# Optimization experiments

Measured on AMD Instinct MI355X. Metric: run time of the kernel, lower is better.

The kernel has to match this reference:

```python
import jax, jax.numpy as jnp
import numpy as np

D_IN = 2048
D_OUT = 2048
NUM_HEADS = 16
HEAD_DIM = D_OUT // NUM_HEADS


def setup_inputs() -> dict:
    key = jax.random.key(0)
    ks = jax.random.split(key, 6)
    b, t = 2, 2048
    x = jax.random.normal(ks[0], (b, t, D_IN), dtype=jnp.float32)
    s = 0.02
    Wq = jax.random.normal(ks[1], (D_OUT, D_IN), dtype=jnp.float32) * s
    Wk = jax.random.normal(ks[2], (D_OUT, D_IN), dtype=jnp.float32) * s
    Wv = jax.random.normal(ks[3], (D_OUT, D_IN), dtype=jnp.float32) * s
    Wo = jax.random.normal(ks[4], (D_OUT, D_OUT), dtype=jnp.float32) * s
    bo = jnp.zeros((D_OUT,), dtype=jnp.float32)
    theta = (10000.0 ** (-jnp.arange(0, HEAD_DIM, 2, dtype=jnp.float32) / HEAD_DIM))
    return {"x": x, "Wq": Wq, "Wk": Wk, "Wv": Wv, "Wo": Wo, "bo": bo, "theta": theta}


def _rope(v, sin, cos):
    # v: [b, t, h, d]; split even/odd feature indices, rotate, concat halves
    ve, vo = v[..., ::2], v[..., 1::2]
    return jnp.concatenate([ve * cos - vo * sin, ve * sin + vo * cos], axis=-1)


def reference(x, Wq, Wk, Wv, Wo, bo, theta):
    b, t, _ = x.shape
    q = (x @ Wq.T).reshape(b, t, NUM_HEADS, HEAD_DIM)
    k = (x @ Wk.T).reshape(b, t, NUM_HEADS, HEAD_DIM)
    v = (x @ Wv.T).reshape(b, t, NUM_HEADS, HEAD_DIM)

    pos = jnp.arange(t, dtype=jnp.float32)[:, None]          # [t, 1]
    freq = pos * theta[None, :]                              # [t, d/2]
    sin = jnp.sin(freq)[None, :, None, :]                    # [1, t, 1, d/2]
    cos = jnp.cos(freq)[None, :, None, :]
    q = _rope(q, sin, cos)
    k = _rope(k, sin, cos)

    # [b, h, t, t]
    scores = jnp.einsum('bqhd,bkhd->bhqk', q, k)
    causal = jnp.triu(jnp.ones((t, t), dtype=bool), k=1)
    scores = jnp.where(causal[None, None], -jnp.inf, scores)
    attn = jax.nn.softmax(scores / jnp.sqrt(jnp.float32(HEAD_DIM)), axis=-1)

    ctx = jnp.einsum('bhqk,bkhd->bqhd', attn, v).reshape(b, t, D_OUT)
    return ctx @ Wo.T + bo
```

## Files before the change

### kernel.cpp

```cpp
#include <hip/hip_runtime.h>

typedef unsigned short ushortT;
typedef short short8 __attribute__((ext_vector_type(8)));
typedef float floatx4 __attribute__((ext_vector_type(4)));

#define D_MODEL 2048
#define HEAD_DIM 128
#define NUM_HEADS 16
#define SEQ 2048
#define BATCH 2
#define M_TOK (BATCH * SEQ)
#define QKV_ELEMS ((size_t)M_TOK * D_MODEL)
#define W_ELEMS ((size_t)D_MODEL * D_MODEL)

__device__ __forceinline__ float bf2f(ushortT h) {
    return __uint_as_float(((unsigned int)h) << 16);
}
__device__ __forceinline__ ushortT f2bf(float f) {
    unsigned int u = __float_as_uint(f);
    u = u + 0x7fffu + ((u >> 16) & 1u);
    return (ushortT)(u >> 16);
}

__device__ __forceinline__ void gload_lds16(const ushortT* g, short* lds_wave_base) {
    __builtin_amdgcn_global_load_lds(
        (const __attribute__((address_space(1))) unsigned int*)g,
        (__attribute__((address_space(3))) unsigned int*)lds_wave_base,
        16, 0, 0);
}

__global__ __launch_bounds__(256) void cvt_all(
    const float* __restrict__ x,  const float* __restrict__ wq,
    const float* __restrict__ wk, const float* __restrict__ wv,
    const float* __restrict__ wo,
    ushortT* __restrict__ xb,  ushortT* __restrict__ wqb,
    ushortT* __restrict__ wkb, ushortT* __restrict__ wvb,
    ushortT* __restrict__ wob)
{
    const size_t XC = QKV_ELEMS / 8;
    const size_t WC = W_ELEMS / 8;
    size_t c = (size_t)blockIdx.x * 256 + threadIdx.x;
    const float* s; ushortT* d;
    if (c < XC)              { s = x;  d = xb;  }
    else if ((c -= XC) < WC) { s = wq; d = wqb; }
    else if ((c -= WC) < WC) { s = wk; d = wkb; }
    else if ((c -= WC) < WC) { s = wv; d = wvb; }
    else     { c -= WC;        s = wo; d = wob; }
    const float* f = s + c * 8;
    floatx4 a = *(const floatx4*)f;
    floatx4 b = *(const floatx4*)(f + 4);
    short8 r;
    r[0] = (short)f2bf(a.x); r[1] = (short)f2bf(a.y);
    r[2] = (short)f2bf(a.z); r[3] = (short)f2bf(a.w);
    r[4] = (short)f2bf(b.x); r[5] = (short)f2bf(b.y);
    r[6] = (short)f2bf(b.z); r[7] = (short)f2bf(b.w);
    *(short8*)(d + c * 8) = r;
}

__global__ __launch_bounds__(256) void sincos_kernel(
    float* __restrict__ tbl, const float* __restrict__ theta)
{
    const int p = blockIdx.x * 256 + threadIdx.x;
    const int t = p >> 6, d = p & 63;
    const float ang = (float)t * theta[d];
    tbl[2 * p]     = sinf(ang);
    tbl[2 * p + 1] = cosf(ang);
}

template<bool OUTF32>
__global__ __launch_bounds__(256) void gemm_bt(
    const ushortT* __restrict__ A,
    const ushortT* __restrict__ W0, const ushortT* __restrict__ W1,
    const ushortT* __restrict__ W2,
    void* C0, void* C1, void* C2, const float* __restrict__ bias)
{
    __shared__ short As[128 * 32];
    __shared__ short Bs[128 * 32];

    const int z = blockIdx.z;
    const ushortT* W = (z == 0) ? W0 : (z == 1 ? W1 : W2);
    void* C = (z == 0) ? C0 : (z == 1 ? C1 : C2);

    const int tid  = threadIdx.x;
    const int wave = tid >> 6;
    const int lane = tid & 63;
    const int lr   = lane & 15;
    const int quad = lane >> 4;
    const int wm   = (wave & 1) * 64;
    const int wn   = (wave >> 1) * 64;

    const int blockM = blockIdx.y * 128;
    const int blockN = blockIdx.x * 128;

    const int srow = tid >> 2;
    const int scol = (tid & 3) * 8;
    const ushortT* ag = A + (size_t)(blockM + srow) * D_MODEL + scol;
    const ushortT* wg = W + (size_t)(blockN + srow) * D_MODEL + scol;
    short* al = As + wave * 512;
    short* bl = Bs + wave * 512;

    floatx4 acc[4][4];
    #pragma unroll
    for (int i = 0; i < 4; i++)
        #pragma unroll
        for (int j = 0; j < 4; j++) acc[i][j] = (floatx4){0.f, 0.f, 0.f, 0.f};

    for (int kk = 0; kk < D_MODEL; kk += 32) {
        gload_lds16(ag + kk,                 al);
        gload_lds16(ag + kk + 64 * D_MODEL,  al + 64 * 32);
        gload_lds16(wg + kk,                 bl);
        gload_lds16(wg + kk + 64 * D_MODEL,  bl + 64 * 32);
        __syncthreads();

        short8 af[4], bf[4];
        #pragma unroll
        for (int s = 0; s < 4; s++) {
            af[s] = *(const short8*)&As[(wm + s * 16 + lr) * 32 + quad * 8];
            bf[s] = *(const short8*)&Bs[(wn + s * 16 + lr) * 32 + quad * 8];
        }
        #pragma unroll
        for (int sm = 0; sm < 4; sm++)
            #pragma unroll
            for (int sn = 0; sn < 4; sn++)
                acc[sm][sn] = __builtin_amdgcn_mfma_f32_16x16x32_bf16(
                    af[sm], bf[sn], acc[sm][sn], 0, 0, 0);
        __syncthreads();
    }

    #pragma unroll
    for (int sm = 0; sm < 4; sm++) {
        const int row = blockM + wm + sm * 16 + quad * 4;
        #pragma unroll
        for (int sn = 0; sn < 4; sn++) {
            const int col = blockN + wn + sn * 16 + lr;
            const float bval = bias ? bias[col] : 0.f;
            #pragma unroll
            for (int rr = 0; rr < 4; rr++) {
                const float val = acc[sm][sn][rr] + bval;
                if constexpr (OUTF32)
                    ((float*)C)[(size_t)(row + rr) * D_MODEL + col] = val;
                else
                    ((ushortT*)C)[(size_t)(row + rr) * D_MODEL + col] = f2bf(val);
            }
        }
    }
}

__global__ __launch_bounds__(256) void kpack_kernel(
    const ushortT* __restrict__ k, ushortT* __restrict__ kf,
    const float* __restrict__ tbl)
{
    const int kt16 = blockIdx.x;
    const int bh   = blockIdx.y;
    const int b = bh >> 4, h = bh & 15;
    const int tid = threadIdx.x;
    const int ks = tid >> 6, lane = tid & 63;
    const int lr = lane & 15, quad = lane >> 4;

    const int t   = kt16 * 16 + lr;
    const int d0  = ks * 32 + quad * 8;
    const int dd0 = d0 & 63;
    const ushortT* src = k + (size_t)(b * SEQ + t) * D_MODEL + h * HEAD_DIM;
    short8 a  = *(const short8*)(src + 2 * dd0);
    short8 b8 = *(const short8*)(src + 2 * dd0 + 8);
    const float* tb = tbl + 2 * ((size_t)t * 64 + dd0);

    short8 v;
    #pragma unroll
    for (int j = 0; j < 8; j++) {
        const float ve = bf2f((ushortT)(j < 4 ? a[2 * j]     : b8[2 * j - 8]));
        const float vo = bf2f((ushortT)(j < 4 ? a[2 * j + 1] : b8[2 * j - 7]));
        const float s = tb[2 * j], c = tb[2 * j + 1];
        v[j] = (short)f2bf((d0 < 64) ? (ve * c - vo * s) : (ve * s + vo * c));
    }
    *(short8*)(kf + ((size_t)(bh * 128 + kt16) * 4 + ks) * 512 + lane * 8) = v;
}

__global__ __launch_bounds__(256) void vpack_kernel(
    const ushortT* __restrict__ v, ushortT* __restrict__ vf)
{
    __shared__ ushortT tile[32][136];
    const int ct = blockIdx.x;
    const int bh = blockIdx.y;
    const int b = bh >> 4, h = bh & 15;
    const int tid = threadIdx.x;

    const int tt = tid >> 3;
    const int dc = (tid & 7) * 16;
    const ushortT* src = v + (size_t)(b * SEQ + ct * 32 + tt) * D_MODEL + h * HEAD_DIM + dc;
    *(short8*)&tile[tt][dc]     = *(const short8*)src;
    *(short8*)&tile[tt][dc + 8] = *(const short8*)(src + 8);
    __syncthreads();

    const int w = tid >> 6, lane = tid & 63;
    const int lr = lane & 15, quad = lane >> 4;
    #pragma unroll
    for (int p = 0; p < 2; p++) {
        const int rt = w + p * 4;
        short8 out;
        #pragma unroll
        for (int j = 0; j < 8; j++)
            out[j] = (short)tile[quad * 8 + j][rt * 16 + lr];
        *(short8*)(vf + ((size_t)(bh * 8 + rt) * 64 + ct) * 512 + lane * 8) = out;
    }
}

__global__ __launch_bounds__(256) void flash_attn2(
    const ushortT* __restrict__ q, const ushortT* __restrict__ kf,
    const ushortT* __restrict__ vf, ushortT* __restrict__ ctx,
    const float* __restrict__ tbl)
{
    __shared__ short Kt[2][16 * 512];
    __shared__ short Vt[2][16 * 512];
    __shared__ short Pl[4][16][72];

    const unsigned lid = blockIdx.x;
    const int xcd  = lid & 7;
    const int slot = lid >> 3;
    const int ih   = slot >> 4;
    const int qtb  = slot & 15;
    const int bh   = (ih << 3) | xcd;

    const int b = bh >> 4, h = bh & 15;
    const size_t base = (size_t)b * SEQ * D_MODEL + h * HEAD_DIM;
    const size_t kfb = (size_t)bh * 128 * 4 * 512;
    const size_t vfb = (size_t)bh * 8 * 64 * 512;
    const int tid = threadIdx.x;
    const int w = tid >> 6, lane = tid & 63;
    const int lr = lane & 15, quad = lane >> 4;
    short* myP = &Pl[w][0][0];

    short8 onesf;
    #pragma unroll
    for (int j = 0; j < 8; j++) onesf[j] = (short)0x3F80;

    auto stage_tile = [&](int kt0, int buf) {
        const ushortT* ksrc = kf + kfb + (size_t)kt0 * 128;
        #pragma unroll
        for (int c = 0; c < 4; c++)
            gload_lds16(ksrc + c * 2048 + tid * 8, &Kt[buf][c * 2048 + w * 512]);
        #pragma unroll
        for (int c = 0; c < 4; c++) {
            const int e    = c * 2048 + tid * 8;
            const int dsub = e >> 10;
            const int rem  = e & 1023;
            const ushortT* vsrc = vf + vfb +
                ((size_t)dsub * 64 + (kt0 >> 5) + (rem >> 9)) * 512 + (rem & 511);
            gload_lds16(vsrc, &Vt[buf][c * 2048 + w * 512]);
        }
    };

    for (int pass = 0; pass < 2; pass++) {
        const int qt = (pass == 0) ? qtb : (SEQ / 64 - 1 - qtb);
        const int q0 = qt * 64 + w * 16;

        short8 Qf[4];
        {
            const ushortT* qrow = q + base + (size_t)(q0 + lr) * D_MODEL;
            const float* trow = tbl + 2 * ((size_t)(q0 + lr) * 64);
            #pragma unroll
            for (int ks = 0; ks < 4; ks++) {
                const int d0  = ks * 32 + quad * 8;
                const int dd0 = d0 & 63;
                short8 a  = *(const short8*)(qrow + 2 * dd0);
                short8 b8 = *(const short8*)(qrow + 2 * dd0 + 8);
                const float* tb = trow + 2 * dd0;
                #pragma unroll
                for (int j = 0; j < 8; j++) {
                    const float ve = bf2f((ushortT)(j < 4 ? a[2 * j]     : b8[2 * j - 8]));
                    const float vo = bf2f((ushortT)(j < 4 ? a[2 * j + 1] : b8[2 * j - 7]));
                    const float s = tb[2 * j], c = tb[2 * j + 1];
                    const float r = (d0 < 64) ? (ve * c - vo * s) : (ve * s + vo * c);
                    Qf[ks][j] = (short)f2bf(r * 0.08838834764831845f);
                }
            }
        }

        floatx4 Of[8];
        #pragma unroll
        for (int i = 0; i < 8; i++) Of[i] = (floatx4){0.f, 0.f, 0.f, 0.f};
        floatx4 lacc = (floatx4){0.f, 0.f, 0.f, 0.f};

        stage_tile(0, 0);
        asm volatile("s_waitcnt vmcnt(0)" ::: "memory");
        __builtin_amdgcn_s_barrier();
        asm volatile("" ::: "memory");

        const int ntiles = qt + 1;
        for (int t = 0; t < ntiles; ++t) {
            const int buf = t & 1;
            const int kt0 = t * 64;

            floatx4 Sf[4];
            #pragma unroll
            for (int sub = 0; sub < 4; sub++) {
                floatx4 acc = {0.f, 0.f, 0.f, 0.f};
                #pragma unroll
                for (int ks = 0; ks < 4; ks++) {
                    short8 Kf_ = *(const short8*)(&Kt[buf][(sub * 4 + ks) * 512 + lane * 8]);
                    acc = __builtin_amdgcn_mfma_f32_16x16x32_bf16(Qf[ks], Kf_, acc, 0, 0, 0);
                }
                Sf[sub] = acc;
            }

            if (kt0 == qt * 64) {
                #pragma unroll
                for (int sub = 0; sub < 4; sub++) {
                    const int ktg = kt0 + sub * 16 + lr;
                    #pragma unroll
                    for (int i = 0; i < 4; i++)
                        if (ktg > q0 + quad * 4 + i) Sf[sub][i] = -1e30f;
                }
            }

            #pragma unroll
            for (int sub = 0; sub < 4; sub++) {
                #pragma unroll
                for (int i = 0; i < 4; i++) {
                    const float p = __expf(fminf(Sf[sub][i], 60.f));
                    myP[(quad * 4 + i) * 72 + sub * 16 + lr] = (short)f2bf(p);
                }
            }

            short8 Vr[16];
            #pragma unroll
            for (int dsub = 0; dsub < 8; dsub++) {
                Vr[2 * dsub]     = *(const short8*)(&Vt[buf][dsub * 1024 + lane * 8]);
                Vr[2 * dsub + 1] = *(const short8*)(&Vt[buf][dsub * 1024 + 512 + lane * 8]);
            }

            if (t + 1 < ntiles) stage_tile((t + 1) * 64, buf ^ 1);

            asm volatile("s_waitcnt lgkmcnt(0)" ::: "memory");
            short8 Pf0 = *(const short8*)(myP + lr * 72 + quad * 8);
            short8 Pf1 = *(const short8*)(myP + lr * 72 + 32 + quad * 8);

            lacc = __builtin_amdgcn_mfma_f32_16x16x32_bf16(Pf0, onesf, lacc, 0, 0, 0);
            lacc = __builtin_amdgcn_mfma_f32_16x16x32_bf16(Pf1, onesf, lacc, 0, 0, 0);

            #pragma unroll
            for (int dsub = 0; dsub < 8; dsub++) {
                Of[dsub] = __builtin_amdgcn_mfma_f32_16x16x32_bf16(
                    Pf0, Vr[2 * dsub], Of[dsub], 0, 0, 0);
                Of[dsub] = __builtin_amdgcn_mfma_f32_16x16x32_bf16(
                    Pf1, Vr[2 * dsub + 1], Of[dsub], 0, 0, 0);
            }

            asm volatile("s_waitcnt vmcnt(0)" ::: "memory");
            __builtin_amdgcn_s_barrier();
            asm volatile("" ::: "memory");
        }

        float inv[4];
        #pragma unroll
        for (int i = 0; i < 4; i++) inv[i] = 1.f / lacc[i];
        #pragma unroll
        for (int dsub = 0; dsub < 8; dsub++)
            #pragma unroll
            for (int i = 0; i < 4; i++)
                ctx[base + (size_t)(q0 + quad * 4 + i) * D_MODEL + dsub * 16 + lr] =
                    f2bf(Of[dsub][i] * inv[i]);
    }
}

extern "C" void kernel_launch(void* const* d_in, const int* in_sizes, int n_in,
                              void* d_out, int out_size, void* d_ws, size_t ws_size,
                              hipStream_t stream) {
    const float* x     = (const float*)d_in[0];
    const float* Wq    = (const float*)d_in[1];
    const float* Wk    = (const float*)d_in[2];
    const float* Wv    = (const float*)d_in[3];
    const float* Wo    = (const float*)d_in[4];
    const float* bo    = (const float*)d_in[5];
    const float* theta = (const float*)d_in[6];

    ushortT* ws  = (ushortT*)d_ws;
    ushortT* qb   = ws;
    ushortT* kb   = ws + QKV_ELEMS;
    ushortT* vb   = ws + 2 * QKV_ELEMS;
    ushortT* kfbp = ws + 3 * QKV_ELEMS;
    ushortT* xb   = kfbp;
    ushortT* wqb  = ws + 4 * QKV_ELEMS;
    ushortT* wkb  = wqb + W_ELEMS;
    ushortT* wvb  = wkb + W_ELEMS;
    ushortT* wob  = wvb + W_ELEMS;
    float*   tbl  = (float*)wvb;

    cvt_all<<<dim3((unsigned)((QKV_ELEMS / 8 + 4 * (W_ELEMS / 8)) / 256)), 256, 0, stream>>>(
        x, Wq, Wk, Wv, Wo, xb, wqb, wkb, wvb, wob);

    gemm_bt<false><<<dim3(D_MODEL / 128, M_TOK / 128, 3), 256, 0, stream>>>(
        xb, wqb, wkb, wvb, qb, kb, vb, nullptr);

    sincos_kernel<<<dim3(SEQ * 64 / 256), 256, 0, stream>>>(tbl, theta);

    kpack_kernel<<<dim3(SEQ / 16, BATCH * NUM_HEADS), 256, 0, stream>>>(kb, kfbp, tbl);

    vpack_kernel<<<dim3(SEQ / 32, BATCH * NUM_HEADS), 256, 0, stream>>>(vb, kb);

    flash_attn2<<<dim3(512), 256, 0, stream>>>(qb, kfbp, kb, vb, tbl);

    gemm_bt<true><<<dim3(D_MODEL / 128, M_TOK / 128, 1), 256, 0, stream>>>(
        vb, wob, wob, wob, d_out, d_out, d_out, bo);
}
```

Measured before the change: 400.4 us.

## Split paired causal q-tile passes into separate blocks and drop double buffering

The attention kernel previously had each block process two query tiles (qtb and its mirror) to balance causal work, with double-buffered K/V staging overlapping loads and compute. It now launches one block per query tile (1024 blocks) and uses single-buffered K/V tiles with a load/sync/compute/sync loop. This halves LDS use per block and raises parallelism, but loses load/compute overlap and the built-in causal load balancing, so blocks have very uneven work.

```diff
diff --git a/kernel.cpp b/kernel.cpp
--- a/kernel.cpp
+++ b/kernel.cpp
@@ -210,15 +210,15 @@
     const ushortT* __restrict__ vf, ushortT* __restrict__ ctx,
     const float* __restrict__ tbl)
 {
-    __shared__ short Kt[2][16 * 512];
-    __shared__ short Vt[2][16 * 512];
+    __shared__ short Kt[16 * 512];
+    __shared__ short Vt[16 * 512];
     __shared__ short Pl[4][16][72];
 
     const unsigned lid = blockIdx.x;
     const int xcd  = lid & 7;
     const int slot = lid >> 3;
-    const int ih   = slot >> 4;
-    const int qtb  = slot & 15;
+    const int ih   = slot >> 5;
+    const int qt   = slot & 31;
     const int bh   = (ih << 3) | xcd;
 
     const int b = bh >> 4, h = bh & 15;
@@ -230,137 +230,121 @@
     const int lr = lane & 15, quad = lane >> 4;
     short* myP = &Pl[w][0][0];
 
+    const int q0 = qt * 64 + w * 16;
+
     short8 onesf;
     #pragma unroll
     for (int j = 0; j < 8; j++) onesf[j] = (short)0x3F80;
 
-    auto stage_tile = [&](int kt0, int buf) {
-        const ushortT* ksrc = kf + kfb + (size_t)kt0 * 128;
-        #pragma unroll
-        for (int c = 0; c < 4; c++)
-            gload_lds16(ksrc + c * 2048 + tid * 8, &Kt[buf][c * 2048 + w * 512]);
-        #pragma unroll
-        for (int c = 0; c < 4; c++) {
-            const int e    = c * 2048 + tid * 8;
-            const int dsub = e >> 10;
-            const int rem  = e & 1023;
-            const ushortT* vsrc = vf + vfb +
-                ((size_t)dsub * 64 + (kt0 >> 5) + (rem >> 9)) * 512 + (rem & 511);
-            gload_lds16(vsrc, &Vt[buf][c * 2048 + w * 512]);
-        }
-    };
-
-    for (int pass = 0; pass < 2; pass++) {
-        const int qt = (pass == 0) ? qtb : (SEQ / 64 - 1 - qtb);
-        const int q0 = qt * 64 + w * 16;
-
-        short8 Qf[4];
+    short8 Qf[4];
+    {
+        const ushortT* qrow = q + base + (size_t)(q0 + lr) * D_MODEL;
+        const float* trow = tbl + 2 * ((size_t)(q0 + lr) * 64);
+        #pragma unroll
+        for (int ks = 0; ks < 4; ks++) {
+            const int d0  = ks * 32 + quad * 8;
+            const int dd0 = d0 & 63;
+            short8 a  = *(const short8*)(qrow + 2 * dd0);
+            short8 b8 = *(const short8*)(qrow + 2 * dd0 + 8);
+            const float* tb = trow + 2 * dd0;
+            #pragma unroll
+            for (int j = 0; j < 8; j++) {
+                const float ve = bf2f((ushortT)(j < 4 ? a[2 * j]     : b8[2 * j - 8]));
+                const float vo = bf2f((ushortT)(j < 4 ? a[2 * j + 1] : b8[2 * j - 7]));
+                const float s = tb[2 * j], c = tb[2 * j + 1];
+                const float r = (d0 < 64) ? (ve * c - vo * s) : (ve * s + vo * c);
+                Qf[ks][j] = (short)f2bf(r * 0.08838834764831845f);
+            }
+        }
+    }
+
+    floatx4 Of[8];
+    #pragma unroll
+    for (int i = 0; i < 8; i++) Of[i] = (floatx4){0.f, 0.f, 0.f, 0.f};
+    floatx4 lacc = (floatx4){0.f, 0.f, 0.f, 0.f};
+
+    for (int kt0 = 0; kt0 <= qt * 64; kt0 += 64) {
         {
-            const ushortT* qrow = q + base + (size_t)(q0 + lr) * D_MODEL;
-            const float* trow = tbl + 2 * ((size_t)(q0 + lr) * 64);
+            const ushortT* ksrc = kf + kfb + (size_t)kt0 * 128;
+            #pragma unroll
+            for (int c = 0; c < 4; c++)
+                gload_lds16(ksrc + c * 2048 + tid * 8, Kt + c * 2048 + w * 512);
+            #pragma unroll
+            for (int c = 0; c < 4; c++) {
+                const int e    = c * 2048 + tid * 8;
+                const int dsub = e >> 10;
+                const int rem  = e & 1023;
+                const ushortT* vsrc = vf + vfb +
+                    ((size_t)dsub * 64 + (kt0 >> 5) + (rem >> 9)) * 512 + (rem & 511);
+                gload_lds16(vsrc, Vt + c * 2048 + w * 512);
+            }
+        }
+        __syncthreads();
+
+        floatx4 Sf[4];
+        #pragma unroll
+        for (int sub = 0; sub < 4; sub++) {
+            floatx4 acc = {0.f, 0.f, 0.f, 0.f};
             #pragma unroll
             for (int ks = 0; ks < 4; ks++) {
-                const int d0  = ks * 32 + quad * 8;
-                const int dd0 = d0 & 63;
-                short8 a  = *(const short8*)(qrow + 2 * dd0);
-                short8 b8 = *(const short8*)(qrow + 2 * dd0 + 8);
-                const float* tb = trow + 2 * dd0;
+                short8 Kf_ = *(const short8*)(Kt + (sub * 4 + ks) * 512 + lane * 8);
+                acc = __builtin_amdgcn_mfma_f32_16x16x32_bf16(Qf[ks], Kf_, acc, 0, 0, 0);
+            }
+            Sf[sub] = acc;
+        }
+
+        if (kt0 == qt * 64) {
+            #pragma unroll
+            for (int sub = 0; sub < 4; sub++) {
+                const int ktg = kt0 + sub * 16 + lr;
                 #pragma unroll
-                for (int j = 0; j < 8; j++) {
-                    const float ve = bf2f((ushortT)(j < 4 ? a[2 * j]     : b8[2 * j - 8]));
-                    const float vo = bf2f((ushortT)(j < 4 ? a[2 * j + 1] : b8[2 * j - 7]));
-                    const float s = tb[2 * j], c = tb[2 * j + 1];
-                    const float r = (d0 < 64) ? (ve * c - vo * s) : (ve * s + vo * c);
-                    Qf[ks][j] = (short)f2bf(r * 0.08838834764831845f);
-                }
-            }
-        }
-
-        floatx4 Of[8];
-        #pragma unroll
-        for (int i = 0; i < 8; i++) Of[i] = (floatx4){0.f, 0.f, 0.f, 0.f};
-        floatx4 lacc = (floatx4){0.f, 0.f, 0.f, 0.f};
-
-        stage_tile(0, 0);
-        asm volatile("s_waitcnt vmcnt(0)" ::: "memory");
-        __builtin_amdgcn_s_barrier();
-        asm volatile("" ::: "memory");
-
-        const int ntiles = qt + 1;
-        for (int t = 0; t < ntiles; ++t) {
-            const int buf = t & 1;
-            const int kt0 = t * 64;
-
-            floatx4 Sf[4];
-            #pragma unroll
-            for (int sub = 0; sub < 4; sub++) {
-                floatx4 acc = {0.f, 0.f, 0.f, 0.f};
-                #pragma unroll
-                for (int ks = 0; ks < 4; ks++) {
-                    short8 Kf_ = *(const short8*)(&Kt[buf][(sub * 4 + ks) * 512 + lane * 8]);
-                    acc = __builtin_amdgcn_mfma_f32_16x16x32_bf16(Qf[ks], Kf_, acc, 0, 0, 0);
-                }
-                Sf[sub] = acc;
-            }
-
-            if (kt0 == qt * 64) {
-                #pragma unroll
-                for (int sub = 0; sub < 4; sub++) {
-                    const int ktg = kt0 + sub * 16 + lr;
-                    #pragma unroll
-                    for (int i = 0; i < 4; i++)
-                        if (ktg > q0 + quad * 4 + i) Sf[sub][i] = -1e30f;
-                }
-            }
-
-            #pragma unroll
-            for (int sub = 0; sub < 4; sub++) {
-                #pragma unroll
-                for (int i = 0; i < 4; i++) {
-                    const float p = __expf(fminf(Sf[sub][i], 60.f));
-                    myP[(quad * 4 + i) * 72 + sub * 16 + lr] = (short)f2bf(p);
-                }
-            }
-
-            short8 Vr[16];
-            #pragma unroll
-            for (int dsub = 0; dsub < 8; dsub++) {
-                Vr[2 * dsub]     = *(const short8*)(&Vt[buf][dsub * 1024 + lane * 8]);
-                Vr[2 * dsub + 1] = *(const short8*)(&Vt[buf][dsub * 1024 + 512 + lane * 8]);
-            }
-
-            if (t + 1 < ntiles) stage_tile((t + 1) * 64, buf ^ 1);
-
-            asm volatile("s_waitcnt lgkmcnt(0)" ::: "memory");
-            short8 Pf0 = *(const short8*)(myP + lr * 72 + quad * 8);
-            short8 Pf1 = *(const short8*)(myP + lr * 72 + 32 + quad * 8);
-
-            lacc = __builtin_amdgcn_mfma_f32_16x16x32_bf16(Pf0, onesf, lacc, 0, 0, 0);
-            lacc = __builtin_amdgcn_mfma_f32_16x16x32_bf16(Pf1, onesf, lacc, 0, 0, 0);
-
-            #pragma unroll
-            for (int dsub = 0; dsub < 8; dsub++) {
-                Of[dsub] = __builtin_amdgcn_mfma_f32_16x16x32_bf16(
-                    Pf0, Vr[2 * dsub], Of[dsub], 0, 0, 0);
-                Of[dsub] = __builtin_amdgcn_mfma_f32_16x16x32_bf16(
-                    Pf1, Vr[2 * dsub + 1], Of[dsub], 0, 0, 0);
-            }
-
-            asm volatile("s_waitcnt vmcnt(0)" ::: "memory");
-            __builtin_amdgcn_s_barrier();
-            asm volatile("" ::: "memory");
-        }
-
-        float inv[4];
-        #pragma unroll
-        for (int i = 0; i < 4; i++) inv[i] = 1.f / lacc[i];
-        #pragma unroll
-        for (int dsub = 0; dsub < 8; dsub++)
-            #pragma unroll
-            for (int i = 0; i < 4; i++)
-                ctx[base + (size_t)(q0 + quad * 4 + i) * D_MODEL + dsub * 16 + lr] =
-                    f2bf(Of[dsub][i] * inv[i]);
-    }
+                for (int i = 0; i < 4; i++)
+                    if (ktg > q0 + quad * 4 + i) Sf[sub][i] = -1e30f;
+            }
+        }
+
+        #pragma unroll
+        for (int sub = 0; sub < 4; sub++) {
+            #pragma unroll
+            for (int i = 0; i < 4; i++) {
+                const float p = __expf(fminf(Sf[sub][i], 60.f));
+                myP[(quad * 4 + i) * 72 + sub * 16 + lr] = (short)f2bf(p);
+            }
+        }
+
+        short8 Vr[16];
+        #pragma unroll
+        for (int dsub = 0; dsub < 8; dsub++) {
+            Vr[2 * dsub]     = *(const short8*)(Vt + dsub * 1024 + lane * 8);
+            Vr[2 * dsub + 1] = *(const short8*)(Vt + dsub * 1024 + 512 + lane * 8);
+        }
+
+        asm volatile("s_waitcnt lgkmcnt(0)" ::: "memory");
+        short8 Pf0 = *(const short8*)(myP + lr * 72 + quad * 8);
+        short8 Pf1 = *(const short8*)(myP + lr * 72 + 32 + quad * 8);
+
+        lacc = __builtin_amdgcn_mfma_f32_16x16x32_bf16(Pf0, onesf, lacc, 0, 0, 0);
+        lacc = __builtin_amdgcn_mfma_f32_16x16x32_bf16(Pf1, onesf, lacc, 0, 0, 0);
+
+        #pragma unroll
+        for (int dsub = 0; dsub < 8; dsub++) {
+            Of[dsub] = __builtin_amdgcn_mfma_f32_16x16x32_bf16(
+                Pf0, Vr[2 * dsub], Of[dsub], 0, 0, 0);
+            Of[dsub] = __builtin_amdgcn_mfma_f32_16x16x32_bf16(
+                Pf1, Vr[2 * dsub + 1], Of[dsub], 0, 0, 0);
+        }
+        __syncthreads();
+    }
+
+    float inv[4];
+    #pragma unroll
+    for (int i = 0; i < 4; i++) inv[i] = 1.f / lacc[i];
+    #pragma unroll
+    for (int dsub = 0; dsub < 8; dsub++)
+        #pragma unroll
+        for (int i = 0; i < 4; i++)
+            ctx[base + (size_t)(q0 + quad * 4 + i) * D_MODEL + dsub * 16 + lr] =
+                f2bf(Of[dsub][i] * inv[i]);
 }
 
 extern "C" void kernel_launch(void* const* d_in, const int* in_sizes, int n_in,
@@ -398,7 +382,7 @@
 
     vpack_kernel<<<dim3(SEQ / 32, BATCH * NUM_HEADS), 256, 0, stream>>>(vb, kb);
 
-    flash_attn2<<<dim3(512), 256, 0, stream>>>(qb, kfbp, kb, vb, tbl);
+    flash_attn2<<<dim3(1024), 256, 0, stream>>>(qb, kfbp, kb, vb, tbl);
 
     gemm_bt<true><<<dim3(D_MODEL / 128, M_TOK / 128, 1), 256, 0, stream>>>(
         vb, wob, wob, wob, d_out, d_out, d_out, bo);
```

After: 441.6 us. +10.3%, slower.
